# Kernel optimization log

Hardware: AMD Instinct MI355X
Metric: run time of the kernel (lower is better)

Reference implementation:

```python
import jax, jax.numpy as jnp
import numpy as np

B, N, D, E, H = 8, 256, 128, 32, 4
HD = D // H
EPS = 1e-5


def setup_inputs() -> dict:
    key = jax.random.key(0)
    ks = jax.random.split(key, 20)
    idx = jnp.arange(N)

    h = jax.random.normal(ks[0], (B, N, D), dtype=jnp.float32)
    adj = (jax.random.uniform(ks[1], (B, N, N)) < 0.5).astype(jnp.float32)
    adj = adj.at[:, idx, idx].set(1.0)
    edge_features = jax.random.normal(ks[2], (B, N, N, E), dtype=jnp.float32)
    src_mask = (jax.random.uniform(ks[3], (B, N, N)) < 0.7).astype(jnp.float32)
    src_mask = src_mask.at[:, idx, idx].set(1.0)

    s = 1.0 / np.sqrt(D)
    se = 1.0 / np.sqrt(E)
    p = {
        "gcn_w": jax.random.normal(ks[4], (D, D)) * s,
        "gcn_b": jnp.zeros((D,)),
        "edge_w": jax.random.normal(ks[5], (D, E)) * se,
        "edge_b": jnp.zeros((D,)),
        "wq": jax.random.normal(ks[6], (D, D)) * s,
        "wk": jax.random.normal(ks[7], (D, D)) * s,
        "wv": jax.random.normal(ks[8], (D, D)) * s,
        "bq": jnp.zeros((D,)),
        "bk": jnp.zeros((D,)),
        "bv": jnp.zeros((D,)),
        "out_w": jax.random.normal(ks[9], (D, D)) * s,
        "out_b": jnp.zeros((D,)),
        "ln_g": jnp.ones((D,)),
        "ln_b": jnp.zeros((D,)),
    }
    return {"h": h, "adj": adj, "edge_features": edge_features, "src_mask": src_mask, **p}


def reference(h, adj, edge_features, src_mask,
              gcn_w, gcn_b, edge_w, edge_b,
              wq, wk, wv, bq, bk, bv, out_w, out_b, ln_g, ln_b):
    b, n, d = h.shape

    # --- GCN branch: degree-normalized aggregation with self-loops ---
    adj_sl = adj + jnp.eye(n, dtype=h.dtype)[None]          # (B,N,N)
    deg = adj_sl.sum(-1, keepdims=True)                      # (B,N,1)
    h_agg = jnp.einsum('bnm,bmd->bnd', adj_sl, h) / deg
    h_gcn = h_agg @ gcn_w.T + gcn_b                          # (B,N,D)

    # --- edge-conditioned key/value: h_ij = h_j + edge_emb ---
    edge_emb = jnp.einsum('bnme,de->bnmd', edge_features, edge_w) + edge_b
    h_ij = h[:, None, :, :] + edge_emb                       # (B,N,N,D)

    # key padding mask: True where edge absent (masked)
    masked = (adj * src_mask) == 0                           # (B,N,N)

    # --- multi-head attention, one query per node ---
    q = (h @ wq.T + bq).reshape(b, n, H, HD)                 # (B,N,H,HD)
    k = (jnp.einsum('bnmd,ed->bnme', h_ij, wk) + bk).reshape(b, n, n, H, HD)
    v = (jnp.einsum('bnmd,ed->bnme', h_ij, wv) + bv).reshape(b, n, n, H, HD)

    scores = jnp.einsum('bnhd,bnmhd->bnhm', q, k) / np.sqrt(HD)  # (B,N,H,N)
    scores = jnp.where(masked[:, :, None, :], -jnp.inf, scores)
    attn = jax.nn.softmax(scores, axis=-1)
    o = jnp.einsum('bnhm,bnmhd->bnhd', attn, v).reshape(b, n, d)
    o = o @ out_w.T + out_b                                  # (B,N,D)

    # residual + layernorm (dropout is identity in eval)
    x = h + o
    mu = x.mean(-1, keepdims=True)
    var = ((x - mu) ** 2).mean(-1, keepdims=True)
    h_attn = ln_g * (x - mu) / jnp.sqrt(var + EPS) + ln_b

    return h_gcn + h_attn
```

## Files before the change

kernel.cpp:

```cpp
#include <hip/hip_runtime.h>
#include <hip/hip_bf16.h>

#define OFF_WKE 0
#define OFF_WVE 4096
#define OFF_KB  8192
#define OFF_VB  8320
#define OFF_QS  8448
#define OFF_HG  270592
#define OFF_K0  532736
#define OFF_V0  663808

static __device__ __forceinline__ float bflo(unsigned int w){
  union { unsigned int u; float f; } x; x.u = w << 16; return x.f;
}
static __device__ __forceinline__ float bfhi(unsigned int w){
  union { unsigned int u; float f; } x; x.u = w & 0xffff0000u; return x.f;
}
static __device__ __forceinline__ unsigned int f2bf(float f){
  union { float f; unsigned int u; } x; x.f = f;
  return (x.u + 0x7fffu + ((x.u >> 16) & 1u)) >> 16;
}

__global__ __launch_bounds__(256) void proj_kernel(
    const float* __restrict__ h, const float* __restrict__ adj,
    const float* __restrict__ gcn_w, const float* __restrict__ gcn_b,
    const float* __restrict__ edge_w, const float* __restrict__ edge_b,
    const float* __restrict__ wq, const float* __restrict__ wk,
    const float* __restrict__ wv, const float* __restrict__ bq,
    const float* __restrict__ bk, const float* __restrict__ bv,
    float* __restrict__ ws)
{
  __shared__ float h_lds[4*128];
  __shared__ float adj_lds[4*256];
  __shared__ float p1[2][4][128];
  __shared__ float p2[2][4][128];
  __shared__ float p3[2][4][128];
  __shared__ float ha_lds[4*132];
  __shared__ float dpart[2][4];

  int t = threadIdx.x;
  int d = t & 127, kh = t >> 7;
  int b = blockIdx.x >> 6;
  int n0 = (blockIdx.x & 63) * 4;
  int r0 = b*256 + n0;

  if (t < 128) ((float4*)h_lds)[t] = ((const float4*)(h + (size_t)r0*128))[t];
  ((float4*)adj_lds)[t] = ((const float4*)(adj + (size_t)r0*256))[t];
  __syncthreads();

  {
    const float4* wq4 = (const float4*)(wq + (size_t)d*128 + kh*64);
    const float4* wk4 = (const float4*)(wk + (size_t)d*128 + kh*64);
    const float4* wv4 = (const float4*)(wv + (size_t)d*128 + kh*64);
    float aq[4]={0,0,0,0}, ak[4]={0,0,0,0}, av[4]={0,0,0,0};
    #pragma unroll
    for (int kk = 0; kk < 16; ++kk) {
      float4 qw = wq4[kk], kw = wk4[kk], vw = wv4[kk];
      int k0 = kh*64 + kk*4;
      #pragma unroll
      for (int i = 0; i < 4; ++i) {
        const float* hr = h_lds + i*128 + k0;
        aq[i] += qw.x*hr[0] + qw.y*hr[1] + qw.z*hr[2] + qw.w*hr[3];
        ak[i] += kw.x*hr[0] + kw.y*hr[1] + kw.z*hr[2] + kw.w*hr[3];
        av[i] += vw.x*hr[0] + vw.y*hr[1] + vw.z*hr[2] + vw.w*hr[3];
      }
    }
    #pragma unroll
    for (int i = 0; i < 4; ++i) { p1[kh][i][d]=aq[i]; p2[kh][i][d]=ak[i]; p3[kh][i][d]=av[i]; }
  }
  __syncthreads();

  unsigned short* K0 = (unsigned short*)(ws + OFF_K0);
  unsigned short* V0 = (unsigned short*)(ws + OFF_V0);
  if (t < 128) {
    const float inv = 0.17677669529663687f;
    #pragma unroll
    for (int i = 0; i < 4; ++i) {
      ws[OFF_QS + (size_t)(r0+i)*128 + d] = (p1[0][i][d] + p1[1][i][d] + bq[d]) * inv;
      K0[(size_t)(r0+i)*128 + d] = (unsigned short)f2bf(p2[0][i][d] + p2[1][i][d]);
      V0[(size_t)(r0+i)*128 + d] = (unsigned short)f2bf(p3[0][i][d] + p3[1][i][d]);
    }
  }
  __syncthreads();

  {
    float ag[4]={0,0,0,0}, dg[4]={0,0,0,0};
    for (int mm = 0; mm < 128; ++mm) {
      int ml = kh*128 + mm;
      float hv = h[((size_t)b*256 + ml)*128 + d];
      #pragma unroll
      for (int i = 0; i < 4; ++i) {
        float a = adj_lds[i*256 + ml] + ((ml == n0 + i) ? 1.0f : 0.0f);
        ag[i] += a * hv;
        dg[i] += a;
      }
    }
    #pragma unroll
    for (int i = 0; i < 4; ++i) p1[kh][i][d] = ag[i];
    if (d == 0) {
      #pragma unroll
      for (int i = 0; i < 4; ++i) dpart[kh][i] = dg[i];
    }
  }
  __syncthreads();
  if (t < 128) {
    #pragma unroll
    for (int i = 0; i < 4; ++i)
      ha_lds[i*132 + d] = (p1[0][i][d] + p1[1][i][d]) / (dpart[0][i] + dpart[1][i]);
  }
  __syncthreads();

  {
    const float4* gw4 = (const float4*)(gcn_w + (size_t)d*128 + kh*64);
    float ga[4]={0,0,0,0};
    #pragma unroll
    for (int kk = 0; kk < 16; ++kk) {
      float4 g4 = gw4[kk];
      int k0 = kh*64 + kk*4;
      #pragma unroll
      for (int i = 0; i < 4; ++i) {
        const float* hr = ha_lds + i*132 + k0;
        ga[i] += g4.x*hr[0] + g4.y*hr[1] + g4.z*hr[2] + g4.w*hr[3];
      }
    }
    #pragma unroll
    for (int i = 0; i < 4; ++i) p2[kh][i][d] = ga[i];
  }
  __syncthreads();
  if (t < 128) {
    #pragma unroll
    for (int i = 0; i < 4; ++i)
      ws[OFF_HG + (size_t)(r0+i)*128 + d] = p2[0][i][d] + p2[1][i][d] + gcn_b[d];
  }

  if (blockIdx.x < 32) {
    int which = blockIdx.x >> 4;
    int e0 = (blockIdx.x & 15) * 256 + t;
    int dd = e0 >> 5, e = e0 & 31;
    const float* W = which ? wv : wk;
    float acc = 0.f;
    #pragma unroll 4
    for (int k2 = 0; k2 < 128; ++k2) acc += W[dd*128+k2] * edge_w[k2*32+e];
    ws[(which ? OFF_WVE : OFF_WKE) + e0] = acc;
  } else if (blockIdx.x == 32) {
    int dd = t & 127;
    const float* W  = (t < 128) ? wk : wv;
    const float* bb = (t < 128) ? bk : bv;
    float acc = bb[dd];
    #pragma unroll 4
    for (int k2 = 0; k2 < 128; ++k2) acc += W[dd*128+k2] * edge_b[k2];
    ws[((t < 128) ? OFF_KB : OFF_VB) + dd] = acc;
  }
}

__global__ __launch_bounds__(256, 5) void attn_kernel(
    const float* __restrict__ edge, const float* __restrict__ adj,
    const float* __restrict__ srcm, const float* __restrict__ h,
    const float* __restrict__ out_w, const float* __restrict__ out_b,
    const float* __restrict__ ln_g, const float* __restrict__ ln_b,
    const float* __restrict__ ws, float* __restrict__ out)
{
  __shared__ unsigned int e_bf[256*18];
  __shared__ float s_lds[1028];
  __shared__ float part4[8*132];
  __shared__ float part5[8*132];
  __shared__ float ebar[128];
  __shared__ float qs_l[128];
  __shared__ float qe_l[128];
  __shared__ float sc_l[4];
  __shared__ float red[8];

  int t  = threadIdx.x;
  int bn = blockIdx.x;
  int b  = bn >> 8;

  {
    const float4* et = (const float4*)(edge + (size_t)bn*8192);
    #pragma unroll
    for (int it = 0; it < 8; ++it) {
      int fi = it*256 + t;
      float4 v = et[fi];
      int row = fi >> 3, c4 = fi & 7;
      uint2 pk;
      pk.x = f2bf(v.x) | (f2bf(v.y) << 16);
      pk.y = f2bf(v.z) | (f2bf(v.w) << 16);
      *(uint2*)(e_bf + row*18 + c4*2) = pk;
    }
  }
  float ma  = adj[(size_t)bn*256 + t];
  float msk = srcm[(size_t)bn*256 + t];
  if (t < 128) qs_l[t] = ws[OFF_QS + (size_t)bn*128 + t];
  __syncthreads();

  if (t < 128) {
    int hh = t >> 5, e = t & 31;
    float acc = 0.f;
    #pragma unroll
    for (int j = 0; j < 32; ++j)
      acc += ws[OFF_WKE + (hh*32 + j)*32 + e] * qs_l[hh*32 + j];
    qe_l[t] = acc;
  } else if (t < 132) {
    int hh = t - 128;
    float acc = 0.f;
    #pragma unroll
    for (int j = 0; j < 32; ++j)
      acc += qs_l[hh*32 + j] * ws[OFF_KB + hh*32 + j];
    sc_l[hh] = acc;
  }
  __syncthreads();

  int m = t;
  float s4[4];
  {
    float e32[32];
    const uint2* er = (const uint2*)(e_bf + m*18);
    #pragma unroll
    for (int j = 0; j < 8; ++j) {
      uint2 w = er[j];
      e32[4*j+0] = bflo(w.x); e32[4*j+1] = bfhi(w.x);
      e32[4*j+2] = bflo(w.y); e32[4*j+3] = bfhi(w.y);
    }
    const uint4* kv = (const uint4*)((const unsigned short*)(ws + OFF_K0)
                                     + (size_t)(b*256 + m)*128);
    #pragma unroll
    for (int hh = 0; hh < 4; ++hh) {
      float acc = sc_l[hh];
      #pragma unroll
      for (int q4 = 0; q4 < 4; ++q4) {
        uint4 kw = kv[hh*4 + q4];
        const float* qp = qs_l + hh*32 + q4*8;
        acc += qp[0]*bflo(kw.x) + qp[1]*bfhi(kw.x)
             + qp[2]*bflo(kw.y) + qp[3]*bfhi(kw.y)
             + qp[4]*bflo(kw.z) + qp[5]*bfhi(kw.z)
             + qp[6]*bflo(kw.w) + qp[7]*bfhi(kw.w);
      }
      const float* qep = qe_l + hh*32;
      #pragma unroll
      for (int j = 0; j < 32; ++j) acc += qep[j]*e32[j];
      s4[hh] = acc;
    }
    if (ma * msk == 0.0f) { s4[0] = s4[1] = s4[2] = s4[3] = -1e30f; }
    #pragma unroll
    for (int hh = 0; hh < 4; ++hh) s_lds[hh*257 + m] = s4[hh];
  }
  __syncthreads();

  {
    int wvh = t >> 6, ln = t & 63;
    float v0 = s_lds[wvh*257 + ln];
    float v1 = s_lds[wvh*257 + ln + 64];
    float v2 = s_lds[wvh*257 + ln + 128];
    float v3 = s_lds[wvh*257 + ln + 192];
    float mx = fmaxf(fmaxf(v0, v1), fmaxf(v2, v3));
    #pragma unroll
    for (int off = 32; off > 0; off >>= 1) mx = fmaxf(mx, __shfl_down(mx, off));
    mx = __shfl(mx, 0);
    float sm = __expf(v0-mx) + __expf(v1-mx) + __expf(v2-mx) + __expf(v3-mx);
    #pragma unroll
    for (int off = 32; off > 0; off >>= 1) sm += __shfl_down(sm, off);
    if (ln == 0) { red[wvh] = mx; red[4+wvh] = 1.0f / sm; }
  }
  __syncthreads();

  #pragma unroll
  for (int hh = 0; hh < 4; ++hh)
    s_lds[hh*257 + m] = __expf(s4[hh] - red[hh]) * red[4+hh];
  __syncthreads();

  {
    int ms  = t >> 5;
    int hh4 = (t >> 3) & 3, e4 = t & 7;
    int c   = t & 31,  hh5 = c >> 3;
    float p4x=0,p4y=0,p4z=0,p4w=0;
    float p5x=0,p5y=0,p5z=0,p5w=0;
    const unsigned int* vrow = (const unsigned int*)(ws + OFF_V0) + (size_t)b*256*64;
    for (int jm = 0; jm < 32; ++jm) {
      int mm = ms*32 + jm;
      float a4 = s_lds[hh4*257 + mm];
      uint2 w = *(const uint2*)(e_bf + mm*18 + e4*2);
      p4x += a4*bflo(w.x); p4y += a4*bfhi(w.x);
      p4z += a4*bflo(w.y); p4w += a4*bfhi(w.y);
      float a5 = s_lds[hh5*257 + mm];
      uint2 vv = *(const uint2*)(vrow + (size_t)mm*64 + c*2);
      p5x += a5*bflo(vv.x); p5y += a5*bfhi(vv.x);
      p5z += a5*bflo(vv.y); p5w += a5*bfhi(vv.y);
    }
    float4 f4; f4.x=p4x; f4.y=p4y; f4.z=p4z; f4.w=p4w;
    *(float4*)(part4 + ms*132 + hh4*32 + e4*4) = f4;
    float4 f5; f5.x=p5x; f5.y=p5y; f5.z=p5z; f5.w=p5w;
    *(float4*)(part5 + ms*132 + c*4) = f5;
  }
  __syncthreads();

  float s2 = 0.f;
  if (t < 128) {
    float se = 0.f;
    #pragma unroll
    for (int g = 0; g < 8; ++g) { se += part4[g*132 + t]; s2 += part5[g*132 + t]; }
    ebar[t] = se;
  }
  __syncthreads();

  if (t < 128) {
    int hh = t >> 5;
    float acc = s2 + ws[OFF_VB + t];
    const float* wve = ws + OFF_WVE + (size_t)t*32;
    #pragma unroll
    for (int e = 0; e < 32; ++e) acc += wve[e] * ebar[hh*32 + e];
    part4[t] = acc;
  }
  float hv = (t < 128) ? h[(size_t)bn*128 + t] : 0.f;
  __syncthreads();

  {
    int d = t & 127, kh = t >> 7;
    const float4* ow4 = (const float4*)(out_w + (size_t)d*128 + kh*64);
    float xa = 0.f;
    #pragma unroll
    for (int kk = 0; kk < 16; ++kk) {
      float4 w4 = ow4[kk];
      const float* op = part4 + kh*64 + kk*4;
      xa += w4.x*op[0] + w4.y*op[1] + w4.z*op[2] + w4.w*op[3];
    }
    part5[kh*128 + d] = xa;
  }
  __syncthreads();

  float x = 0.f;
  if (t < 128) {
    x = part5[t] + part5[128 + t] + out_b[t] + hv;
    part4[256 + t] = x;
  }
  __syncthreads();

  if (t < 64) {
    float x0 = part4[256 + t], x1 = part4[256 + t + 64];
    float s = x0 + x1, ss = x0*x0 + x1*x1;
    #pragma unroll
    for (int off = 32; off > 0; off >>= 1) {
      s  += __shfl_down(s,  off);
      ss += __shfl_down(ss, off);
    }
    if (t == 0) {
      float mu = s * (1.0f/128.0f);
      red[0] = mu;
      red[1] = rsqrtf(ss * (1.0f/128.0f) - mu*mu + 1e-5f);
    }
  }
  __syncthreads();

  if (t < 128) {
    float mu = red[0], rs = red[1];
    out[(size_t)bn*128 + t] =
        ln_g[t]*(x - mu)*rs + ln_b[t] + ws[OFF_HG + (size_t)bn*128 + t];
  }
}

extern "C" void kernel_launch(void* const* d_in, const int* in_sizes, int n_in,
                              void* d_out, int out_size, void* d_ws, size_t ws_size,
                              hipStream_t stream) {
  (void)in_sizes; (void)n_in; (void)out_size; (void)ws_size;
  const float* h     = (const float*)d_in[0];
  const float* adj   = (const float*)d_in[1];
  const float* edge  = (const float*)d_in[2];
  const float* srcm  = (const float*)d_in[3];
  const float* gcn_w = (const float*)d_in[4];
  const float* gcn_b = (const float*)d_in[5];
  const float* edge_w= (const float*)d_in[6];
  const float* edge_b= (const float*)d_in[7];
  const float* wq    = (const float*)d_in[8];
  const float* wk    = (const float*)d_in[9];
  const float* wv    = (const float*)d_in[10];
  const float* bq    = (const float*)d_in[11];
  const float* bk    = (const float*)d_in[12];
  const float* bv    = (const float*)d_in[13];
  const float* out_w = (const float*)d_in[14];
  const float* out_b = (const float*)d_in[15];
  const float* ln_g  = (const float*)d_in[16];
  const float* ln_b  = (const float*)d_in[17];

  float* ws  = (float*)d_ws;
  float* out = (float*)d_out;

  proj_kernel<<<512, 256, 0, stream>>>(h, adj, gcn_w, gcn_b, edge_w, edge_b,
                                       wq, wk, wv, bq, bk, bv, ws);
  attn_kernel<<<2048, 256, 0, stream>>>(edge, adj, srcm, h, out_w, out_b,
                                        ln_g, ln_b, ws, out);
}
```

Measured before the change: 206.3 us.

## Add weight-transpose prep kernel, move q·We projection to proj, drop softmax max pass

Adds a prep kernel that transposes wq/wk/wv/out_w/gcn_w into the workspace so that projection loads are coalesced across threads. The per-query q·W_ke and bias scores move from the attention kernel into proj_kernel, which now handles two rows per block across 1024 blocks. The attention kernel redistributes score work so four threads cover the four heads of each key, and it fuses the mask into exp. It skips max subtraction and folds the softmax normalization into the final accumulations, which removes two barriers and a reduction pass. The risk is overflow in exp when scores are large, plus one extra kernel launch and a lower occupancy hint.

```diff
diff --git a/kernel.cpp b/kernel.cpp
--- a/kernel.cpp
+++ b/kernel.cpp
@@ -1,14 +1,21 @@
 #include <hip/hip_runtime.h>
 #include <hip/hip_bf16.h>
 
-#define OFF_WKE 0
-#define OFF_WVE 4096
-#define OFF_KB  8192
-#define OFF_VB  8320
-#define OFF_QS  8448
-#define OFF_HG  270592
-#define OFF_K0  532736
-#define OFF_V0  663808
+#define OFF_WQT 0
+#define OFF_WKT 16384
+#define OFF_WVT 32768
+#define OFF_OWT 49152
+#define OFF_GWT 65536
+#define OFF_WKE 81920
+#define OFF_WVET 86016
+#define OFF_KB  90112
+#define OFF_VB  90240
+#define OFF_SC  90368
+#define OFF_QS  98560
+#define OFF_QE  360704
+#define OFF_HG  622848
+#define OFF_K0  884992
+#define OFF_V0  1016064
 
 static __device__ __forceinline__ float bflo(unsigned int w){
   union { unsigned int u; float f; } x; x.u = w << 16; return x.f;
@@ -21,128 +28,34 @@
   return (x.u + 0x7fffu + ((x.u >> 16) & 1u)) >> 16;
 }
 
-__global__ __launch_bounds__(256) void proj_kernel(
-    const float* __restrict__ h, const float* __restrict__ adj,
-    const float* __restrict__ gcn_w, const float* __restrict__ gcn_b,
-    const float* __restrict__ edge_w, const float* __restrict__ edge_b,
+__global__ __launch_bounds__(256) void prep_kernel(
     const float* __restrict__ wq, const float* __restrict__ wk,
-    const float* __restrict__ wv, const float* __restrict__ bq,
-    const float* __restrict__ bk, const float* __restrict__ bv,
-    float* __restrict__ ws)
+    const float* __restrict__ wv, const float* __restrict__ out_w,
+    const float* __restrict__ gcn_w, const float* __restrict__ edge_w,
+    const float* __restrict__ edge_b, const float* __restrict__ bk,
+    const float* __restrict__ bv, float* __restrict__ ws)
 {
-  __shared__ float h_lds[4*128];
-  __shared__ float adj_lds[4*256];
-  __shared__ float p1[2][4][128];
-  __shared__ float p2[2][4][128];
-  __shared__ float p3[2][4][128];
-  __shared__ float ha_lds[4*132];
-  __shared__ float dpart[2][4];
-
-  int t = threadIdx.x;
-  int d = t & 127, kh = t >> 7;
-  int b = blockIdx.x >> 6;
-  int n0 = (blockIdx.x & 63) * 4;
-  int r0 = b*256 + n0;
-
-  if (t < 128) ((float4*)h_lds)[t] = ((const float4*)(h + (size_t)r0*128))[t];
-  ((float4*)adj_lds)[t] = ((const float4*)(adj + (size_t)r0*256))[t];
-  __syncthreads();
-
-  {
-    const float4* wq4 = (const float4*)(wq + (size_t)d*128 + kh*64);
-    const float4* wk4 = (const float4*)(wk + (size_t)d*128 + kh*64);
-    const float4* wv4 = (const float4*)(wv + (size_t)d*128 + kh*64);
-    float aq[4]={0,0,0,0}, ak[4]={0,0,0,0}, av[4]={0,0,0,0};
-    #pragma unroll
-    for (int kk = 0; kk < 16; ++kk) {
-      float4 qw = wq4[kk], kw = wk4[kk], vw = wv4[kk];
-      int k0 = kh*64 + kk*4;
-      #pragma unroll
-      for (int i = 0; i < 4; ++i) {
-        const float* hr = h_lds + i*128 + k0;
-        aq[i] += qw.x*hr[0] + qw.y*hr[1] + qw.z*hr[2] + qw.w*hr[3];
-        ak[i] += kw.x*hr[0] + kw.y*hr[1] + kw.z*hr[2] + kw.w*hr[3];
-        av[i] += vw.x*hr[0] + vw.y*hr[1] + vw.z*hr[2] + vw.w*hr[3];
-      }
-    }
-    #pragma unroll
-    for (int i = 0; i < 4; ++i) { p1[kh][i][d]=aq[i]; p2[kh][i][d]=ak[i]; p3[kh][i][d]=av[i]; }
-  }
-  __syncthreads();
-
-  unsigned short* K0 = (unsigned short*)(ws + OFF_K0);
-  unsigned short* V0 = (unsigned short*)(ws + OFF_V0);
-  if (t < 128) {
-    const float inv = 0.17677669529663687f;
-    #pragma unroll
-    for (int i = 0; i < 4; ++i) {
-      ws[OFF_QS + (size_t)(r0+i)*128 + d] = (p1[0][i][d] + p1[1][i][d] + bq[d]) * inv;
-      K0[(size_t)(r0+i)*128 + d] = (unsigned short)f2bf(p2[0][i][d] + p2[1][i][d]);
-      V0[(size_t)(r0+i)*128 + d] = (unsigned short)f2bf(p3[0][i][d] + p3[1][i][d]);
-    }
-  }
-  __syncthreads();
-
-  {
-    float ag[4]={0,0,0,0}, dg[4]={0,0,0,0};
-    for (int mm = 0; mm < 128; ++mm) {
-      int ml = kh*128 + mm;
-      float hv = h[((size_t)b*256 + ml)*128 + d];
-      #pragma unroll
-      for (int i = 0; i < 4; ++i) {
-        float a = adj_lds[i*256 + ml] + ((ml == n0 + i) ? 1.0f : 0.0f);
-        ag[i] += a * hv;
-        dg[i] += a;
-      }
-    }
-    #pragma unroll
-    for (int i = 0; i < 4; ++i) p1[kh][i][d] = ag[i];
-    if (d == 0) {
-      #pragma unroll
-      for (int i = 0; i < 4; ++i) dpart[kh][i] = dg[i];
-    }
-  }
-  __syncthreads();
-  if (t < 128) {
-    #pragma unroll
-    for (int i = 0; i < 4; ++i)
-      ha_lds[i*132 + d] = (p1[0][i][d] + p1[1][i][d]) / (dpart[0][i] + dpart[1][i]);
-  }
-  __syncthreads();
-
-  {
-    const float4* gw4 = (const float4*)(gcn_w + (size_t)d*128 + kh*64);
-    float ga[4]={0,0,0,0};
-    #pragma unroll
-    for (int kk = 0; kk < 16; ++kk) {
-      float4 g4 = gw4[kk];
-      int k0 = kh*64 + kk*4;
-      #pragma unroll
-      for (int i = 0; i < 4; ++i) {
-        const float* hr = ha_lds + i*132 + k0;
-        ga[i] += g4.x*hr[0] + g4.y*hr[1] + g4.z*hr[2] + g4.w*hr[3];
-      }
-    }
-    #pragma unroll
-    for (int i = 0; i < 4; ++i) p2[kh][i][d] = ga[i];
-  }
-  __syncthreads();
-  if (t < 128) {
-    #pragma unroll
-    for (int i = 0; i < 4; ++i)
-      ws[OFF_HG + (size_t)(r0+i)*128 + d] = p2[0][i][d] + p2[1][i][d] + gcn_b[d];
-  }
-
-  if (blockIdx.x < 32) {
-    int which = blockIdx.x >> 4;
-    int e0 = (blockIdx.x & 15) * 256 + t;
+  int blk = blockIdx.x, t = threadIdx.x;
+  if (blk < 320) {
+    int w = blk >> 6;
+    int e0 = (blk & 63) * 256 + t;
+    const float* src = (w==0) ? wq : (w==1) ? wk : (w==2) ? wv : (w==3) ? out_w : gcn_w;
+    float* dst = ws + ((w==0) ? OFF_WQT : (w==1) ? OFF_WKT : (w==2) ? OFF_WVT
+                      : (w==3) ? OFF_OWT : OFF_GWT);
+    int k = e0 >> 7, d = e0 & 127;
+    dst[e0] = src[d*128 + k];
+  } else if (blk < 352) {
+    int idx = blk - 320;
+    int which = idx >> 4;
+    int e0 = (idx & 15) * 256 + t;
     int dd = e0 >> 5, e = e0 & 31;
     const float* W = which ? wv : wk;
     float acc = 0.f;
     #pragma unroll 4
     for (int k2 = 0; k2 < 128; ++k2) acc += W[dd*128+k2] * edge_w[k2*32+e];
-    ws[(which ? OFF_WVE : OFF_WKE) + e0] = acc;
-  } else if (blockIdx.x == 32) {
+    if (which) ws[OFF_WVET + e*128 + dd] = acc;
+    else       ws[OFF_WKE + e0] = acc;
+  } else {
     int dd = t & 127;
     const float* W  = (t < 128) ? wk : wv;
     const float* bb = (t < 128) ? bk : bv;
@@ -153,22 +66,135 @@
   }
 }
 
-__global__ __launch_bounds__(256, 5) void attn_kernel(
+__global__ __launch_bounds__(256) void proj_kernel(
+    const float* __restrict__ h, const float* __restrict__ adj,
+    const float* __restrict__ bq, const float* __restrict__ gcn_b,
+    float* __restrict__ ws)
+{
+  __shared__ float h_lds[256];
+  __shared__ float adj_lds[512];
+  __shared__ float p1[2][2][128];
+  __shared__ float p2[2][2][128];
+  __shared__ float p3[2][2][128];
+  __shared__ float qrow[2*132];
+  __shared__ float dpart[2][2];
+  __shared__ float ha_lds[2*132];
+
+  int t = threadIdx.x;
+  int d = t & 127, kh = t >> 7;
+  int r0 = blockIdx.x * 2;
+  int b  = r0 >> 8, n0 = r0 & 255;
+
+  if (t < 64)  ((float4*)h_lds)[t]   = ((const float4*)(h   + (size_t)r0*128))[t];
+  if (t < 128) ((float4*)adj_lds)[t] = ((const float4*)(adj + (size_t)r0*256))[t];
+  __syncthreads();
+
+  {
+    const float* wqT = ws + OFF_WQT;
+    const float* wkT = ws + OFF_WKT;
+    const float* wvT = ws + OFF_WVT;
+    float aq0=0,aq1=0,ak0=0,ak1=0,av0=0,av1=0;
+    #pragma unroll 4
+    for (int kk = 0; kk < 64; ++kk) {
+      int k = kh*64 + kk;
+      float qw = wqT[k*128+d], kw = wkT[k*128+d], vw = wvT[k*128+d];
+      float h0 = h_lds[k], h1 = h_lds[128+k];
+      aq0 += qw*h0; aq1 += qw*h1;
+      ak0 += kw*h0; ak1 += kw*h1;
+      av0 += vw*h0; av1 += vw*h1;
+    }
+    p1[kh][0][d]=aq0; p1[kh][1][d]=aq1;
+    p2[kh][0][d]=ak0; p2[kh][1][d]=ak1;
+    p3[kh][0][d]=av0; p3[kh][1][d]=av1;
+  }
+  __syncthreads();
+
+  {
+    unsigned short* K0 = (unsigned short*)(ws + OFF_K0);
+    unsigned short* V0 = (unsigned short*)(ws + OFF_V0);
+    int i = t >> 7, dd = t & 127;
+    const float inv = 0.17677669529663687f;
+    float q = (p1[0][i][dd] + p1[1][i][dd] + bq[dd]) * inv;
+    ws[OFF_QS + (size_t)(r0+i)*128 + dd] = q;
+    qrow[i*132 + dd] = q;
+    K0[(size_t)(r0+i)*128 + dd] = (unsigned short)f2bf(p2[0][i][dd] + p2[1][i][dd]);
+    V0[(size_t)(r0+i)*128 + dd] = (unsigned short)f2bf(p3[0][i][dd] + p3[1][i][dd]);
+  }
+  __syncthreads();
+
+  {
+    float ag0=0, ag1=0, dg0=0, dg1=0;
+    #pragma unroll 4
+    for (int mm = 0; mm < 128; ++mm) {
+      int ml = kh*128 + mm;
+      float hv = h[((size_t)b*256 + ml)*128 + d];
+      float a0 = adj_lds[ml]       + ((ml == n0)     ? 1.0f : 0.0f);
+      float a1 = adj_lds[256 + ml] + ((ml == n0 + 1) ? 1.0f : 0.0f);
+      ag0 += a0*hv; ag1 += a1*hv; dg0 += a0; dg1 += a1;
+    }
+    p1[kh][0][d]=ag0; p1[kh][1][d]=ag1;
+    if (d == 0) { dpart[kh][0]=dg0; dpart[kh][1]=dg1; }
+  }
+  {
+    int i = t >> 7, he = t & 127, hh = he >> 5, e = he & 31;
+    float acc = 0.f;
+    #pragma unroll
+    for (int j = 0; j < 32; ++j)
+      acc += ws[OFF_WKE + (hh*32 + j)*32 + e] * qrow[i*132 + hh*32 + j];
+    ws[OFF_QE + (size_t)(r0+i)*128 + he] = acc;
+  }
+  if (t < 8) {
+    int i = t >> 2, hh = t & 3;
+    float acc = 0.f;
+    #pragma unroll
+    for (int j = 0; j < 32; ++j)
+      acc += qrow[i*132 + hh*32 + j] * ws[OFF_KB + hh*32 + j];
+    ws[OFF_SC + (size_t)(r0+i)*4 + hh] = acc;
+  }
+  __syncthreads();
+
+  {
+    int i = t >> 7, dd = t & 127;
+    ha_lds[i*132 + dd] = (p1[0][i][dd] + p1[1][i][dd]) / (dpart[0][i] + dpart[1][i]);
+  }
+  __syncthreads();
+
+  {
+    const float* gwT = ws + OFF_GWT;
+    float g0=0, g1=0;
+    #pragma unroll 4
+    for (int kk = 0; kk < 64; ++kk) {
+      int k = kh*64 + kk;
+      float gw = gwT[k*128+d];
+      g0 += gw * ha_lds[k];
+      g1 += gw * ha_lds[132 + k];
+    }
+    p2[kh][0][d]=g0; p2[kh][1][d]=g1;
+  }
+  __syncthreads();
+  {
+    int i = t >> 7, dd = t & 127;
+    ws[OFF_HG + (size_t)(r0+i)*128 + dd] = p2[0][i][dd] + p2[1][i][dd] + gcn_b[dd];
+  }
+}
+
+__global__ __launch_bounds__(256, 4) void attn_kernel(
     const float* __restrict__ edge, const float* __restrict__ adj,
     const float* __restrict__ srcm, const float* __restrict__ h,
-    const float* __restrict__ out_w, const float* __restrict__ out_b,
-    const float* __restrict__ ln_g, const float* __restrict__ ln_b,
-    const float* __restrict__ ws, float* __restrict__ out)
+    const float* __restrict__ out_b, const float* __restrict__ ln_g,
+    const float* __restrict__ ln_b, const float* __restrict__ ws,
+    float* __restrict__ out)
 {
   __shared__ unsigned int e_bf[256*18];
-  __shared__ float s_lds[1028];
+  __shared__ float s_lds[4*264];
   __shared__ float part4[8*132];
   __shared__ float part5[8*132];
+  __shared__ float qs_l[132];
+  __shared__ float qe_l[132];
+  __shared__ float sc_l[4];
   __shared__ float ebar[128];
-  __shared__ float qs_l[128];
-  __shared__ float qe_l[128];
-  __shared__ float sc_l[4];
-  __shared__ float red[8];
+  __shared__ float wpart[16];
+  __shared__ float red[2];
 
   int t  = threadIdx.x;
   int bn = blockIdx.x;
@@ -186,108 +212,87 @@
       pk.y = f2bf(v.z) | (f2bf(v.w) << 16);
       *(uint2*)(e_bf + row*18 + c4*2) = pk;
     }
-  }
-  float ma  = adj[(size_t)bn*256 + t];
-  float msk = srcm[(size_t)bn*256 + t];
-  if (t < 128) qs_l[t] = ws[OFF_QS + (size_t)bn*128 + t];
-  __syncthreads();
-
-  if (t < 128) {
-    int hh = t >> 5, e = t & 31;
-    float acc = 0.f;
-    #pragma unroll
-    for (int j = 0; j < 32; ++j)
-      acc += ws[OFF_WKE + (hh*32 + j)*32 + e] * qs_l[hh*32 + j];
-    qe_l[t] = acc;
-  } else if (t < 132) {
-    int hh = t - 128;
-    float acc = 0.f;
-    #pragma unroll
-    for (int j = 0; j < 32; ++j)
-      acc += qs_l[hh*32 + j] * ws[OFF_KB + hh*32 + j];
-    sc_l[hh] = acc;
-  }
-  __syncthreads();
-
-  int m = t;
-  float s4[4];
-  {
-    float e32[32];
-    const uint2* er = (const uint2*)(e_bf + m*18);
-    #pragma unroll
-    for (int j = 0; j < 8; ++j) {
-      uint2 w = er[j];
-      e32[4*j+0] = bflo(w.x); e32[4*j+1] = bfhi(w.x);
-      e32[4*j+2] = bflo(w.y); e32[4*j+3] = bfhi(w.y);
-    }
-    const uint4* kv = (const uint4*)((const unsigned short*)(ws + OFF_K0)
-                                     + (size_t)(b*256 + m)*128);
-    #pragma unroll
-    for (int hh = 0; hh < 4; ++hh) {
+    float mp = adj[(size_t)bn*256 + t] * srcm[(size_t)bn*256 + t];
+    e_bf[t*18 + 16] = __float_as_uint(mp);
+    if (t < 128) {
+      int hh = t >> 5, j = t & 31;
+      qs_l[hh*33 + j] = ws[OFF_QS + (size_t)bn*128 + t];
+      qe_l[hh*33 + j] = ws[OFF_QE + (size_t)bn*128 + t];
+    }
+    if (t < 4) sc_l[t] = ws[OFF_SC + (size_t)bn*4 + t];
+  }
+  __syncthreads();
+
+  int hh = t & 3;
+  {
+    const float* qp  = qs_l + hh*33;
+    const float* qep = qe_l + hh*33;
+    float exsum = 0.f;
+    const unsigned short* K0 = (const unsigned short*)(ws + OFF_K0) + (size_t)b*256*128;
+    #pragma unroll 2
+    for (int pass = 0; pass < 4; ++pass) {
+      int mm = (pass << 6) | (t >> 2);
+      const uint4* kv = (const uint4*)(K0 + (size_t)mm*128) + hh*4;
       float acc = sc_l[hh];
       #pragma unroll
       for (int q4 = 0; q4 < 4; ++q4) {
-        uint4 kw = kv[hh*4 + q4];
-        const float* qp = qs_l + hh*32 + q4*8;
-        acc += qp[0]*bflo(kw.x) + qp[1]*bfhi(kw.x)
-             + qp[2]*bflo(kw.y) + qp[3]*bfhi(kw.y)
-             + qp[4]*bflo(kw.z) + qp[5]*bfhi(kw.z)
-             + qp[6]*bflo(kw.w) + qp[7]*bfhi(kw.w);
+        uint4 kw = kv[q4];
+        const float* qq = qp + q4*8;
+        acc += qq[0]*bflo(kw.x) + qq[1]*bfhi(kw.x)
+             + qq[2]*bflo(kw.y) + qq[3]*bfhi(kw.y)
+             + qq[4]*bflo(kw.z) + qq[5]*bfhi(kw.z)
+             + qq[6]*bflo(kw.w) + qq[7]*bfhi(kw.w);
       }
-      const float* qep = qe_l + hh*32;
+      const uint2* er = (const uint2*)(e_bf + mm*18);
       #pragma unroll
-      for (int j = 0; j < 32; ++j) acc += qep[j]*e32[j];
-      s4[hh] = acc;
-    }
-    if (ma * msk == 0.0f) { s4[0] = s4[1] = s4[2] = s4[3] = -1e30f; }
-    #pragma unroll
-    for (int hh = 0; hh < 4; ++hh) s_lds[hh*257 + m] = s4[hh];
-  }
-  __syncthreads();
-
-  {
-    int wvh = t >> 6, ln = t & 63;
-    float v0 = s_lds[wvh*257 + ln];
-    float v1 = s_lds[wvh*257 + ln + 64];
-    float v2 = s_lds[wvh*257 + ln + 128];
-    float v3 = s_lds[wvh*257 + ln + 192];
-    float mx = fmaxf(fmaxf(v0, v1), fmaxf(v2, v3));
-    #pragma unroll
-    for (int off = 32; off > 0; off >>= 1) mx = fmaxf(mx, __shfl_down(mx, off));
-    mx = __shfl(mx, 0);
-    float sm = __expf(v0-mx) + __expf(v1-mx) + __expf(v2-mx) + __expf(v3-mx);
-    #pragma unroll
-    for (int off = 32; off > 0; off >>= 1) sm += __shfl_down(sm, off);
-    if (ln == 0) { red[wvh] = mx; red[4+wvh] = 1.0f / sm; }
-  }
-  __syncthreads();
-
-  #pragma unroll
-  for (int hh = 0; hh < 4; ++hh)
-    s_lds[hh*257 + m] = __expf(s4[hh] - red[hh]) * red[4+hh];
-  __syncthreads();
-
-  {
+      for (int j = 0; j < 8; ++j) {
+        uint2 w = er[j];
+        acc += qep[4*j+0]*bflo(w.x) + qep[4*j+1]*bfhi(w.x)
+             + qep[4*j+2]*bflo(w.y) + qep[4*j+3]*bfhi(w.y);
+      }
+      float mp = __uint_as_float(e_bf[mm*18 + 16]);
+      float ex = (mp == 0.0f) ? 0.0f : __expf(acc);
+      s_lds[hh*264 + mm] = ex;
+      exsum += ex;
+    }
+    exsum += __shfl_down(exsum, 4);
+    exsum += __shfl_down(exsum, 8);
+    exsum += __shfl_down(exsum, 16);
+    exsum += __shfl_down(exsum, 32);
+    if ((t & 63) < 4) wpart[(t >> 6)*4 + hh] = exsum;
+  }
+  __syncthreads();
+
+  {
+    float s0 = wpart[0]+wpart[4]+wpart[8]+wpart[12];
+    float s1 = wpart[1]+wpart[5]+wpart[9]+wpart[13];
+    float s2h = wpart[2]+wpart[6]+wpart[10]+wpart[14];
+    float s3h = wpart[3]+wpart[7]+wpart[11]+wpart[15];
+
     int ms  = t >> 5;
     int hh4 = (t >> 3) & 3, e4 = t & 7;
     int c   = t & 31,  hh5 = c >> 3;
+    float sum4 = (hh4==0)?s0:(hh4==1)?s1:(hh4==2)?s2h:s3h;
+    float sum5 = (hh5==0)?s0:(hh5==1)?s1:(hh5==2)?s2h:s3h;
+    float inv4 = 1.0f / sum4, inv5 = 1.0f / sum5;
+
     float p4x=0,p4y=0,p4z=0,p4w=0;
     float p5x=0,p5y=0,p5z=0,p5w=0;
     const unsigned int* vrow = (const unsigned int*)(ws + OFF_V0) + (size_t)b*256*64;
     for (int jm = 0; jm < 32; ++jm) {
       int mm = ms*32 + jm;
-      float a4 = s_lds[hh4*257 + mm];
+      float a4 = s_lds[hh4*264 + mm];
       uint2 w = *(const uint2*)(e_bf + mm*18 + e4*2);
       p4x += a4*bflo(w.x); p4y += a4*bfhi(w.x);
       p4z += a4*bflo(w.y); p4w += a4*bfhi(w.y);
-      float a5 = s_lds[hh5*257 + mm];
+      float a5 = s_lds[hh5*264 + mm];
       uint2 vv = *(const uint2*)(vrow + (size_t)mm*64 + c*2);
       p5x += a5*bflo(vv.x); p5y += a5*bfhi(vv.x);
       p5z += a5*bflo(vv.y); p5w += a5*bfhi(vv.y);
     }
-    float4 f4; f4.x=p4x; f4.y=p4y; f4.z=p4z; f4.w=p4w;
+    float4 f4; f4.x=p4x*inv4; f4.y=p4y*inv4; f4.z=p4z*inv4; f4.w=p4w*inv4;
     *(float4*)(part4 + ms*132 + hh4*32 + e4*4) = f4;
-    float4 f5; f5.x=p5x; f5.y=p5y; f5.z=p5z; f5.w=p5w;
+    float4 f5; f5.x=p5x*inv5; f5.y=p5y*inv5; f5.z=p5z*inv5; f5.w=p5w*inv5;
     *(float4*)(part5 + ms*132 + c*4) = f5;
   }
   __syncthreads();
@@ -301,40 +306,31 @@
   }
   __syncthreads();
 
+  float hv = 0.f;
   if (t < 128) {
-    int hh = t >> 5;
+    int hd = t >> 5;
     float acc = s2 + ws[OFF_VB + t];
-    const float* wve = ws + OFF_WVE + (size_t)t*32;
-    #pragma unroll
-    for (int e = 0; e < 32; ++e) acc += wve[e] * ebar[hh*32 + e];
+    const float* wveT = ws + OFF_WVET;
+    #pragma unroll 4
+    for (int e = 0; e < 32; ++e) acc += wveT[e*128 + t] * ebar[hd*32 + e];
     part4[t] = acc;
-  }
-  float hv = (t < 128) ? h[(size_t)bn*128 + t] : 0.f;
-  __syncthreads();
-
-  {
-    int d = t & 127, kh = t >> 7;
-    const float4* ow4 = (const float4*)(out_w + (size_t)d*128 + kh*64);
-    float xa = 0.f;
-    #pragma unroll
-    for (int kk = 0; kk < 16; ++kk) {
-      float4 w4 = ow4[kk];
-      const float* op = part4 + kh*64 + kk*4;
-      xa += w4.x*op[0] + w4.y*op[1] + w4.z*op[2] + w4.w*op[3];
-    }
-    part5[kh*128 + d] = xa;
+    hv = h[(size_t)bn*128 + t];
   }
   __syncthreads();
 
   float x = 0.f;
   if (t < 128) {
-    x = part5[t] + part5[128 + t] + out_b[t] + hv;
-    part4[256 + t] = x;
+    const float* owT = ws + OFF_OWT;
+    float acc = out_b[t] + hv;
+    #pragma unroll 8
+    for (int k = 0; k < 128; ++k) acc += owT[k*128 + t] * part4[k];
+    x = acc;
+    part4[132 + t] = x;
   }
   __syncthreads();
 
   if (t < 64) {
-    float x0 = part4[256 + t], x1 = part4[256 + t + 64];
+    float x0 = part4[132 + t], x1 = part4[132 + t + 64];
     float s = x0 + x1, ss = x0*x0 + x1*x1;
     #pragma unroll
     for (int off = 32; off > 0; off >>= 1) {
@@ -382,8 +378,7 @@
   float* ws  = (float*)d_ws;
   float* out = (float*)d_out;
 
-  proj_kernel<<<512, 256, 0, stream>>>(h, adj, gcn_w, gcn_b, edge_w, edge_b,
-                                       wq, wk, wv, bq, bk, bv, ws);
-  attn_kernel<<<2048, 256, 0, stream>>>(edge, adj, srcm, h, out_w, out_b,
-                                        ln_g, ln_b, ws, out);
-}
+  prep_kernel<<<353, 256, 0, stream>>>(wq, wk, wv, out_w, gcn_w, edge_w, edge_b, bk, bv, ws);
+  proj_kernel<<<1024, 256, 0, stream>>>(h, adj, bq, gcn_b, ws);
+  attn_kernel<<<2048, 256, 0, stream>>>(edge, adj, srcm, h, out_b, ln_g, ln_b, ws, out);
+}
```

Result: faster. 189.0 us (-8.4%).
